# Performance work log

Hardware: AMD Instinct MI355X
Metric: run time of the kernel (lower is better)

Reference implementation:

```python
import jax, jax.numpy as jnp
import numpy as np

T, B, C = 2048, 8, 512
OUT = 512
NE = 16
TOPK = 2
LOSS_SCALE = 0.01
NEG_INF = 1.0e6  # module uses -1000000.0 for masked logits


def setup_inputs() -> dict:
    key = jax.random.key(0)
    k = jax.random.split(key, 4)
    a_assign = np.sqrt(6.0 / (C + NE)).astype(np.float32)  # xavier_uniform for Linear(C, NE)
    a_w1 = np.float32(np.sqrt(6.0) / (C + OUT))            # dynamic_init_method == 1
    return {
        "x": jax.random.normal(k[0], (T, B, C), dtype=jnp.float32),
        "assign_w": jax.random.uniform(k[1], (NE, C), minval=-a_assign, maxval=a_assign, dtype=jnp.float32),
        "assign_b": jnp.zeros((NE,), dtype=jnp.float32),
        "pw_w1": jax.random.uniform(k[2], (NE, OUT * C), minval=-a_w1, maxval=a_w1, dtype=jnp.float32),
        "bias_w": jnp.zeros((OUT, C), dtype=jnp.float32),  # pw_bias weight initialized to 0
        "bias_b": jnp.zeros((OUT,), dtype=jnp.float32),
    }


def reference(x, assign_w, assign_b, pw_w1, bias_w, bias_b):
    # key=None path of ConditionalDLFactorized18.forward, eval mode, tau=0 -> softmax gating.
    tokens = x.reshape(T * B, C)
    # Gating energies: Linear(key_dim, ne)
    energies = tokens @ assign_w.T + assign_b  # [TB, ne]
    # keeptopk_masked: set entries below k-th largest to -1e6
    topv, _ = jax.lax.top_k(energies, TOPK)
    energies = jnp.where(energies < topv[..., TOPK - 1:TOPK], -NEG_INF, energies)
    resp = jax.nn.softmax(energies, axis=-1)  # [TB, ne]
    # Importance/commitment loss (torch.std is unbiased -> ddof=1)
    importance = resp.sum(axis=0)  # [ne]
    loss = (LOSS_SCALE * jnp.std(importance, ddof=1) / jnp.mean(importance)).reshape(1)
    # Algebraically-equivalent reorder of (resp @ pw_w1).view(T,B,out,in) @ x:
    # apply each expert's matrix to the token first, then mix with resp.
    W = pw_w1.reshape(NE, OUT, C)
    expert_out = jnp.einsum("nc,eoc->neo", tokens, W)      # [TB, ne, out]
    y = jnp.einsum("ne,neo->no", resp, expert_out)          # [TB, out]
    y = y.reshape(T, B, OUT)
    # dynamic bias: pw_bias(x0) = x0 @ bias_w.T + bias_b
    y = y + x @ bias_w.T + bias_b
    return y, loss
```

## Files before the change

### kernel.cpp

```cpp
#include <hip/hip_runtime.h>
#include <hip/hip_bf16.h>

#define TB 16384
#define CDIM 512
#define OUTD 512
#define NE 16
#define NE_TOT 17
#define LOSS_SCALE 0.01f
#define BM 256
#define BN 128
#define BK 32
#define NSTEP 16
#define MAX_SCHED 80
#define MAXFLAG 8192
#define MARGIN 1e-3f

typedef __bf16 bf16_t;
typedef bf16_t bf16x8 __attribute__((ext_vector_type(8)));
typedef float f32x4 __attribute__((ext_vector_type(4)));
typedef unsigned short ushort4_t __attribute__((ext_vector_type(4)));
typedef unsigned short ushort8_t __attribute__((ext_vector_type(8)));

__device__ __forceinline__ unsigned short f2bf(float f) {
    unsigned int u = __float_as_uint(f);
    u += 0x7fffu + ((u >> 16) & 1u);
    return (unsigned short)(u >> 16);
}
__device__ __forceinline__ float bf2f(unsigned short h) {
    return __uint_as_float((unsigned int)h << 16);
}
__device__ __forceinline__ int sw4(int r) { return (r ^ (r >> 2)) & 3; }

__device__ __forceinline__ void async_copy16(void* lds, const void* g) {
    __builtin_amdgcn_global_load_lds(
        (const __attribute__((address_space(1))) unsigned int*)g,
        (__attribute__((address_space(3))) unsigned int*)lds, 16, 0, 0);
}

__global__ __launch_bounds__(256) void k_prep(
    const float* __restrict__ aw, unsigned short* __restrict__ awhl,
    int* cnt0, int* cnt1, float* importance, int* nflag, int* wflag)
{
    int t = threadIdx.x;
    if (t < NE) { cnt0[t] = 0; cnt1[t] = 0; importance[t] = 0.f; }
    if (t == 0) { *nflag = 0; *wflag = 0; }
    for (int i = t; i < NE * CDIM; i += 256) {
        float f = aw[i];
        unsigned short h = f2bf(f);
        float r = f - bf2f(h);
        awhl[i] = h;
        awhl[NE * CDIM + i] = f2bf(r);
    }
}

__global__ void k_wconv(const float* __restrict__ pw, const float* __restrict__ bw,
                        unsigned short* __restrict__ wbf, int* __restrict__ wflag) {
    long i = (long)blockIdx.x * 256 + threadIdx.x;
    const long NPW = (long)NE * OUTD * CDIM / 4;
    const long NTOT = (long)NE_TOT * OUTD * CDIM / 4;
    if (i >= NTOT) return;
    const float* src = (i < NPW) ? (pw + i * 4) : (bw + (i - NPW) * 4);
    float4 v = *(const float4*)src;
    ushort4_t o;
    o[0] = f2bf(v.x); o[1] = f2bf(v.y); o[2] = f2bf(v.z); o[3] = f2bf(v.w);
    long row = i >> 7;
    int e0 = (int)(i & 127) * 4;
    int kt = e0 >> 5;
    int cc = (e0 >> 3) & 3;
    int half = e0 & 7;
    int ccs = cc ^ sw4((int)(row & 15));
    *(ushort4_t*)(wbf + row * CDIM + kt * 32 + ccs * 8 + half) = o;
    if (i >= NPW && (v.x != 0.f || v.y != 0.f || v.z != 0.f || v.w != 0.f))
        atomicOr(wflag, 1);
}

__global__ __launch_bounds__(256) void k_gate(
    const float* __restrict__ x, const unsigned short* __restrict__ awhl,
    const float* __restrict__ ab, unsigned short* __restrict__ xbf,
    int* __restrict__ dec, float2* __restrict__ respd,
    int* __restrict__ flaglist, int* __restrict__ nflag, float* __restrict__ importance,
    int* __restrict__ cnt0, int* __restrict__ cnt1)
{
    __shared__ float imp_s[NE];
    __shared__ int c0_s[NE], c1_s[NE];
    int tid = threadIdx.x;
    if (tid < NE) { imp_s[tid] = 0.f; c0_s[tid] = 0; c1_s[tid] = 0; }
    __syncthreads();

    int wv = tid >> 6, l = tid & 63;
    int n0 = blockIdx.x * 64 + wv * 16;
    int e = l & 15;
    int kg = l >> 4;

    const float* xrow = x + (size_t)(n0 + e) * CDIM + kg * 8;
    unsigned short* xbrow = xbf + (size_t)(n0 + e) * CDIM + kg * 8;
    const unsigned short* whiP = awhl + e * CDIM + kg * 8;
    const unsigned short* wloP = whiP + NE * CDIM;

    f32x4 acc = (f32x4){0.f, 0.f, 0.f, 0.f};
    #pragma unroll 4
    for (int ks = 0; ks < 16; ++ks) {
        float4 v0 = *(const float4*)(xrow + ks * 32);
        float4 v1 = *(const float4*)(xrow + ks * 32 + 4);
        ushort8_t hx, lx;
        #define CVT(idx, f) { unsigned short h_ = f2bf(f); hx[idx] = h_; \
                              float r_ = (f) - bf2f(h_); lx[idx] = f2bf(r_); }
        CVT(0, v0.x) CVT(1, v0.y) CVT(2, v0.z) CVT(3, v0.w)
        CVT(4, v1.x) CVT(5, v1.y) CVT(6, v1.z) CVT(7, v1.w)
        #undef CVT
        *(ushort8_t*)(xbrow + ks * 32) = hx;
        ushort8_t wh8 = *(const ushort8_t*)(whiP + ks * 32);
        ushort8_t wl8 = *(const ushort8_t*)(wloP + ks * 32);
        bf16x8 ah = *(bf16x8*)&hx, al = *(bf16x8*)&lx;
        bf16x8 bh = *(bf16x8*)&wh8, bl = *(bf16x8*)&wl8;
        acc = __builtin_amdgcn_mfma_f32_16x16x32_bf16(al, bh, acc, 0, 0, 0);
        acc = __builtin_amdgcn_mfma_f32_16x16x32_bf16(ah, bl, acc, 0, 0, 0);
        acc = __builtin_amdgcn_mfma_f32_16x16x32_bf16(ah, bh, acc, 0, 0, 0);
    }
    float bias = ab[e];
    f32x4 E;
    #pragma unroll
    for (int q = 0; q < 4; ++q) E[q] = acc[q] + bias;

    f32x4 m1 = E, m2, m3;
    #pragma unroll
    for (int q = 0; q < 4; ++q) { m2[q] = -3.4e38f; m3[q] = -3.4e38f; }
    #pragma unroll
    for (int off = 1; off <= 8; off <<= 1) {
        #pragma unroll
        for (int q = 0; q < 4; ++q) {
            float o1 = __shfl_xor(m1[q], off, 64);
            float o2 = __shfl_xor(m2[q], off, 64);
            float o3 = __shfl_xor(m3[q], off, 64);
            float M1 = fmaxf(m1[q], o1), x1 = fminf(m1[q], o1);
            float h2 = fmaxf(m2[q], o2), l2 = fminf(m2[q], o2);
            float M2 = fmaxf(x1, h2), x2 = fminf(x1, h2);
            float M3 = fmaxf(fmaxf(x2, l2), fmaxf(m3[q], o3));
            m1[q] = M1; m2[q] = M2; m3[q] = M3;
        }
    }
    f32x4 p, z;
    #pragma unroll
    for (int q = 0; q < 4; ++q) p[q] = (E[q] >= m2[q]) ? expf(E[q] - m1[q]) : 0.f;
    z = p;
    #pragma unroll
    for (int off = 1; off <= 8; off <<= 1)
        #pragma unroll
        for (int q = 0; q < 4; ++q) z[q] += __shfl_xor(z[q], off, 64);
    f32x4 resp;
    #pragma unroll
    for (int q = 0; q < 4; ++q) resp[q] = p[q] / z[q];

    int grp = l >> 4;
    int elo_q[4], ehi_q[4];
    float rlo_q[4], rhi_q[4];
    #pragma unroll
    for (int q = 0; q < 4; ++q) {
        unsigned long long mq = __ballot(p[q] > 0.f);
        unsigned int sub = (unsigned int)((mq >> (grp * 16)) & 0xffffULL);
        elo_q[q] = __builtin_ctz(sub);
        ehi_q[q] = 31 - __builtin_clz(sub);
        rlo_q[q] = __shfl(resp[q], grp * 16 + elo_q[q], 64);
        rhi_q[q] = __shfl(resp[q], grp * 16 + ehi_q[q], 64);
    }
    if ((l & 15) == 0) {
        #pragma unroll
        for (int q = 0; q < 4; ++q) {
            int n = n0 + grp * 4 + q;
            dec[n] = elo_q[q] | (ehi_q[q] << 8);
            respd[n] = make_float2(rlo_q[q], rhi_q[q]);
            atomicAdd(&c0_s[elo_q[q]], 1);
            atomicAdd(&c1_s[ehi_q[q]], 1);
            if (m2[q] - m3[q] < MARGIN) {
                int ix = atomicAdd(nflag, 1);
                if (ix < MAXFLAG) flaglist[ix] = n;
            }
        }
    }
    float s = resp[0] + resp[1] + resp[2] + resp[3];
    s += __shfl_xor(s, 16, 64);
    s += __shfl_xor(s, 32, 64);
    if (l < 16) atomicAdd(&imp_s[e], s);
    __syncthreads();
    if (tid < NE) {
        unsafeAtomicAdd(&importance[tid], imp_s[tid]);
        if (c0_s[tid]) atomicAdd(&cnt0[tid], c0_s[tid]);
        if (c1_s[tid]) atomicAdd(&cnt1[tid], c1_s[tid]);
    }
}

__global__ __launch_bounds__(256) void k_repair(
    const float* __restrict__ x, const float* __restrict__ aw, const float* __restrict__ ab,
    const int* __restrict__ flaglist, const int* __restrict__ nflag,
    int* __restrict__ dec, float2* __restrict__ respd, float* __restrict__ importance,
    int* __restrict__ cnt0, int* __restrict__ cnt1)
{
    __shared__ double part[16][17];
    __shared__ double Ed[16];
    int tid = threadIdx.x;
    int e = tid >> 4, p = tid & 15;
    int nf = *nflag; if (nf > MAXFLAG) nf = MAXFLAG;
    for (int fi = blockIdx.x; fi < nf; fi += gridDim.x) {
        int n = flaglist[fi];
        const float* xp_ = x + (size_t)n * CDIM + p * 32;
        const float* wp = aw + e * CDIM + p * 32;
        double acc = 0.0;
        for (int j = 0; j < 32; ++j) acc = fma((double)xp_[j], (double)wp[j], acc);
        part[e][p] = acc;
        __syncthreads();
        if (tid < 16) {
            double s = (double)ab[tid];
            for (int q = 0; q < 16; ++q) s += part[tid][q];
            Ed[tid] = s;
        }
        __syncthreads();
        if (tid == 0) {
            double m1 = -1e300, m2 = -1e300, m3 = -1e300;
            for (int q = 0; q < 16; ++q) {
                double v = Ed[q];
                if (v > m1) { m3 = m2; m2 = m1; m1 = v; }
                else if (v > m2) { m3 = m2; m2 = v; }
                else if (v > m3) { m3 = v; }
            }
            int elo = -1, ehi = -1;
            for (int q = 0; q < 16; ++q)
                if (Ed[q] >= m2) { if (elo < 0) elo = q; else ehi = q; }
            double plo = exp(Ed[elo] - m1), phi = exp(Ed[ehi] - m1);
            double zz = plo + phi;
            float rlo = (float)(plo / zz), rhi = (float)(phi / zz);
            int od = dec[n]; float2 orr = respd[n];
            int oelo = od & 0xff, oehi = (od >> 8) & 0xff;
            unsafeAtomicAdd(&importance[oelo], -orr.x);
            unsafeAtomicAdd(&importance[oehi], -orr.y);
            unsafeAtomicAdd(&importance[elo], rlo);
            unsafeAtomicAdd(&importance[ehi], rhi);
            if (oelo != elo) { atomicSub(&cnt0[oelo], 1); atomicAdd(&cnt0[elo], 1); }
            if (oehi != ehi) { atomicSub(&cnt1[oehi], 1); atomicAdd(&cnt1[ehi], 1); }
            dec[n] = elo | (ehi << 8);
            respd[n] = make_float2(rlo, rhi);
        }
        __syncthreads();
    }
}

__global__ void k_finish(const float* __restrict__ importance, float* __restrict__ out_loss,
                         const int* __restrict__ cnt0, const int* __restrict__ cnt1,
                         int* __restrict__ fill0, int* __restrict__ fill1,
                         int* __restrict__ end0a, int* __restrict__ end1a,
                         int* __restrict__ sched0, int* __restrict__ sched1,
                         int* __restrict__ sn0, int* __restrict__ sn1) {
    int l = threadIdx.x;
    if (l < 64) {
        float v = (l < NE) ? importance[l] : 0.f;
        float s = v;
        #pragma unroll
        for (int off = 8; off >= 1; off >>= 1) s += __shfl_xor(s, off, 64);
        float mean = s / 16.f;
        float d = (l < NE) ? (v - mean) : 0.f;
        float ss = d * d;
        #pragma unroll
        for (int off = 8; off >= 1; off >>= 1) ss += __shfl_xor(ss, off, 64);
        if (l == 0) {
            float stdv = sqrtf(ss / 15.f);
            out_loss[0] = LOSS_SCALE * stdv / mean;
        }
    } else if (l == 64) {
        int p = 0, base = 0;
        for (int e = 0; e < NE; ++e) {
            fill0[e] = base;
            end0a[e] = base + cnt0[e];
            int nb = (cnt0[e] + BM - 1) / BM;
            for (int i = 0; i < nb; ++i) sched0[p++] = (e << 20) | (base + i * BM);
            base += cnt0[e];
        }
        *sn0 = p;
    } else if (l == 65) {
        int p = 0, base = 0;
        for (int e = 0; e < NE; ++e) {
            fill1[e] = base;
            end1a[e] = base + cnt1[e];
            int nb = (cnt1[e] + BM - 1) / BM;
            for (int i = 0; i < nb; ++i) sched1[p++] = (e << 20) | (base + i * BM);
            base += cnt1[e];
        }
        *sn1 = p;
    }
}

__global__ __launch_bounds__(256) void k_scatter(
    const int* __restrict__ dec, int* __restrict__ fill0, int* __restrict__ fill1,
    int* __restrict__ idx0c, int* __restrict__ idx1c)
{
    __shared__ int l0[NE], l1[NE], b0[NE], b1[NE];
    int tid = threadIdx.x;
    if (tid < NE) { l0[tid] = 0; l1[tid] = 0; }
    __syncthreads();
    int n = blockIdx.x * 256 + tid;
    int d = dec[n];
    int elo = d & 0xff, ehi = (d >> 8) & 0xff;
    int p0 = atomicAdd(&l0[elo], 1);
    int p1 = atomicAdd(&l1[ehi], 1);
    __syncthreads();
    if (tid < NE) {
        b0[tid] = atomicAdd(&fill0[tid], l0[tid]);
        b1[tid] = atomicAdd(&fill1[tid], l1[tid]);
    }
    __syncthreads();
    idx0c[b0[elo] + p0] = n;
    idx1c[b1[ehi] + p1] = n;
}

template<int MODE>
__global__ __launch_bounds__(512) void k_gemm(
    const unsigned short* __restrict__ xbf, const unsigned short* __restrict__ wbf,
    const int* __restrict__ idxc, const float2* __restrict__ respd,
    const int* __restrict__ sched, const int* __restrict__ sn,
    const int* __restrict__ enda, const int* __restrict__ wflag,
    const float* __restrict__ bias_b, float* __restrict__ y)
{
    int e, m0, end;
    if (MODE == 2) {
        if (*wflag == 0) return;
        e = NE; m0 = blockIdx.x * BM; end = TB;
    } else {
        if ((int)blockIdx.x >= *sn) return;
        int s = sched[blockIdx.x];
        e = s >> 20; m0 = s & 0xFFFFF; end = enda[e];
    }
    int n0 = blockIdx.y * BN;
    int tid = threadIdx.x;
    int wave = tid >> 6, lane = tid & 63;
    int wm = wave >> 1, wn = wave & 1;
    int fr = lane & 15, fq = lane >> 4;

    __shared__ unsigned short As[2][BM * BK];
    __shared__ unsigned short Bs[2][BN * BK];

    f32x4 acc[4][4];
    #pragma unroll
    for (int m = 0; m < 4; ++m)
        #pragma unroll
        for (int nn = 0; nn < 4; ++nn) acc[m][nn] = (f32x4){0.f, 0.f, 0.f, 0.f};

    int rl = lane >> 2, cc = lane & 3;
    const unsigned short* aS[2];
    #pragma unroll
    for (int c = 0; c < 2; ++c) {
        int rloc = wave * 32 + c * 16 + rl;
        int tokr;
        if (MODE == 2) tokr = m0 + rloc;
        else { int rr = m0 + rloc; if (rr >= end) rr = end - 1; tokr = idxc[rr]; }
        aS[c] = xbf + (size_t)tokr * CDIM + (cc ^ sw4(rloc)) * 8;
    }
    const unsigned short* bS =
        wbf + ((size_t)e * OUTD + n0 + wave * 16 + rl) * CDIM + cc * 8;

    auto stage = [&](int buf, int t) {
        async_copy16(&As[buf][(wave * 32) * BK], aS[0] + t * BK);
        async_copy16(&As[buf][(wave * 32 + 16) * BK], aS[1] + t * BK);
        async_copy16(&Bs[buf][(wave * 16) * BK], bS + t * BK);
    };
    auto compute = [&](int cb) {
        bf16x8 af[4], bv[4];
        #pragma unroll
        for (int m = 0; m < 4; ++m) {
            int row = wm * 64 + m * 16 + fr;
            af[m] = *(const bf16x8*)(&As[cb][row * BK + ((fq ^ sw4(fr)) * 8)]);
        }
        #pragma unroll
        for (int nn = 0; nn < 4; ++nn) {
            int row = wn * 64 + nn * 16 + fr;
            bv[nn] = *(const bf16x8*)(&Bs[cb][row * BK + ((fq ^ sw4(fr)) * 8)]);
        }
        #pragma unroll
        for (int m = 0; m < 4; ++m)
            #pragma unroll
            for (int nn = 0; nn < 4; ++nn)
                acc[m][nn] = __builtin_amdgcn_mfma_f32_16x16x32_bf16(af[m], bv[nn], acc[m][nn], 0, 0, 0);
    };

    stage(0, 0); stage(1, 1);
    #pragma unroll
    for (int t = 0; t < NSTEP; ++t) {
        if (t < NSTEP - 1) asm volatile("s_waitcnt vmcnt(3)" ::: "memory");
        else               asm volatile("s_waitcnt vmcnt(0)" ::: "memory");
        __builtin_amdgcn_sched_barrier(0);
        __builtin_amdgcn_s_barrier();
        asm volatile("" ::: "memory");
        compute(t & 1);
        __builtin_amdgcn_s_barrier();
        asm volatile("" ::: "memory");
        if (t + 2 < NSTEP) stage(t & 1, t + 2);
    }

    float bb[4];
    if (MODE == 0) {
        #pragma unroll
        for (int nn = 0; nn < 4; ++nn) bb[nn] = bias_b[n0 + wn * 64 + nn * 16 + fr];
    }
    #pragma unroll
    for (int m = 0; m < 4; ++m)
        #pragma unroll
        for (int q = 0; q < 4; ++q) {
            int r = m0 + wm * 64 + m * 16 + fq * 4 + q;
            if (r < end) {
                int tok = (MODE == 2) ? r : idxc[r];
                float w = 1.f;
                if (MODE != 2) {
                    float2 rp = respd[tok];
                    w = (MODE == 0) ? rp.x : rp.y;
                }
                float* yrow = y + (size_t)tok * OUTD + n0 + wn * 64 + fr;
                #pragma unroll
                for (int nn = 0; nn < 4; ++nn) {
                    if (MODE == 0)      yrow[nn * 16] = fmaf(w, acc[m][nn][q], bb[nn]);
                    else if (MODE == 1) yrow[nn * 16] += w * acc[m][nn][q];
                    else                yrow[nn * 16] += acc[m][nn][q];
                }
            }
        }
}

extern "C" void kernel_launch(void* const* d_in, const int* in_sizes, int n_in,
                              void* d_out, int out_size, void* d_ws, size_t ws_size,
                              hipStream_t stream) {
    const float* x        = (const float*)d_in[0];
    const float* assign_w = (const float*)d_in[1];
    const float* assign_b = (const float*)d_in[2];
    const float* pw_w1    = (const float*)d_in[3];
    const float* bias_w   = (const float*)d_in[4];
    const float* bias_b   = (const float*)d_in[5];
    float* y    = (float*)d_out;
    float* loss = y + (size_t)TB * OUTD;

    char* ws = (char*)d_ws;
    unsigned short* wbf  = (unsigned short*)(ws);
    unsigned short* xbf  = (unsigned short*)(ws + 8912896);
    int*    idx0c     = (int*)   (ws + 25690112);
    int*    idx1c     = (int*)   (ws + 25755648);
    int*    dec       = (int*)   (ws + 25821184);
    float2* respd     = (float2*)(ws + 25886720);
    int*    flaglist  = (int*)   (ws + 26017792);
    unsigned short* awhl = (unsigned short*)(ws + 26050560);
    char*   misc      = ws + 26083328;
    int*    cnt0      = (int*)   (misc + 0);
    int*    cnt1      = (int*)   (misc + 64);
    int*    fill0     = (int*)   (misc + 128);
    int*    fill1     = (int*)   (misc + 192);
    int*    end0a     = (int*)   (misc + 256);
    int*    end1a     = (int*)   (misc + 320);
    float*  importance= (float*) (misc + 384);
    int*    nflag     = (int*)   (misc + 448);
    int*    wflag     = (int*)   (misc + 452);
    int*    sn0       = (int*)   (misc + 456);
    int*    sn1       = (int*)   (misc + 460);
    int*    sched0    = (int*)   (misc + 512);
    int*    sched1    = (int*)   (misc + 832);

    k_prep<<<1, 256, 0, stream>>>(assign_w, awhl, cnt0, cnt1, importance, nflag, wflag);
    k_wconv<<<(NE_TOT * OUTD * CDIM / 4 + 255) / 256, 256, 0, stream>>>(pw_w1, bias_w, wbf, wflag);
    k_gate<<<TB / 64, 256, 0, stream>>>(x, awhl, assign_b, xbf, dec, respd,
                                        flaglist, nflag, importance, cnt0, cnt1);
    k_repair<<<32, 256, 0, stream>>>(x, assign_w, assign_b, flaglist, nflag,
                                     dec, respd, importance, cnt0, cnt1);
    k_finish<<<1, 128, 0, stream>>>(importance, loss, cnt0, cnt1, fill0, fill1,
                                    end0a, end1a, sched0, sched1, sn0, sn1);
    k_scatter<<<TB / 256, 256, 0, stream>>>(dec, fill0, fill1, idx0c, idx1c);
    k_gemm<0><<<dim3(MAX_SCHED, OUTD / BN), 512, 0, stream>>>(
        xbf, wbf, idx0c, respd, sched0, sn0, end0a, wflag, bias_b, y);
    k_gemm<1><<<dim3(MAX_SCHED, OUTD / BN), 512, 0, stream>>>(
        xbf, wbf, idx1c, respd, sched1, sn1, end1a, wflag, bias_b, y);
    k_gemm<2><<<dim3(TB / BM, OUTD / BN), 512, 0, stream>>>(
        xbf, wbf, idx1c, respd, sched1, sn1, end1a, wflag, bias_b, y);
}
```

Before: 111.5 us.

## Fuse top-1 and top-2 expert GEMMs into one launch with atomic ordering

Replaces the two separate grouped-GEMM launches (first and second routed expert) with one kernel. Blocks alternate between the two ranks. Second-rank blocks compute their tile and then spin on a global counter until every first-rank block has written its output, and only then do their read-modify-write accumulate. This lets the two GEMM phases overlap and removes one launch and its tail. The dense bias GEMM moves into its own specialised kernel. The risks are idle spinning blocks holding compute units, and possible deadlock if waiting blocks fill every slot before all first-rank blocks are scheduled.

Measured after the change: 299.9 us. +169.1%, slower.

```diff
diff --git a/kernel.cpp b/kernel.cpp
--- a/kernel.cpp
+++ b/kernel.cpp
@@ -39,11 +39,11 @@
 
 __global__ __launch_bounds__(256) void k_prep(
     const float* __restrict__ aw, unsigned short* __restrict__ awhl,
-    int* cnt0, int* cnt1, float* importance, int* nflag, int* wflag)
+    int* cnt0, int* cnt1, float* importance, int* nflag, int* wflag, int* done0)
 {
     int t = threadIdx.x;
     if (t < NE) { cnt0[t] = 0; cnt1[t] = 0; importance[t] = 0.f; }
-    if (t == 0) { *nflag = 0; *wflag = 0; }
+    if (t == 0) { *nflag = 0; *wflag = 0; *done0 = 0; }
     for (int i = t; i < NE * CDIM; i += 256) {
         float f = aw[i];
         unsigned short h = f2bf(f);
@@ -310,23 +310,24 @@
     idx1c[b1[ehi] + p1] = n;
 }
 
-template<int MODE>
-__global__ __launch_bounds__(512) void k_gemm(
+__global__ __launch_bounds__(512) void k_moe(
     const unsigned short* __restrict__ xbf, const unsigned short* __restrict__ wbf,
-    const int* __restrict__ idxc, const float2* __restrict__ respd,
-    const int* __restrict__ sched, const int* __restrict__ sn,
-    const int* __restrict__ enda, const int* __restrict__ wflag,
-    const float* __restrict__ bias_b, float* __restrict__ y)
+    const int* __restrict__ idx0c, const int* __restrict__ idx1c,
+    const float2* __restrict__ respd,
+    const int* __restrict__ sched0, const int* __restrict__ sched1,
+    const int* __restrict__ sn0, const int* __restrict__ sn1,
+    const int* __restrict__ end0a, const int* __restrict__ end1a,
+    const float* __restrict__ bias_b, float* __restrict__ y, int* __restrict__ done0)
 {
-    int e, m0, end;
-    if (MODE == 2) {
-        if (*wflag == 0) return;
-        e = NE; m0 = blockIdx.x * BM; end = TB;
-    } else {
-        if ((int)blockIdx.x >= *sn) return;
-        int s = sched[blockIdx.x];
-        e = s >> 20; m0 = s & 0xFFFFF; end = enda[e];
-    }
+    int rank = blockIdx.x & 1;
+    int six = blockIdx.x >> 1;
+    const int* sched = rank ? sched1 : sched0;
+    const int* idxc  = rank ? idx1c  : idx0c;
+    const int* enda  = rank ? end1a  : end0a;
+    int sn = rank ? *sn1 : *sn0;
+    if (six >= sn) return;
+    int s = sched[six];
+    int e = s >> 20, m0 = s & 0xFFFFF, end = enda[e];
     int n0 = blockIdx.y * BN;
     int tid = threadIdx.x;
     int wave = tid >> 6, lane = tid & 63;
@@ -347,10 +348,8 @@
     #pragma unroll
     for (int c = 0; c < 2; ++c) {
         int rloc = wave * 32 + c * 16 + rl;
-        int tokr;
-        if (MODE == 2) tokr = m0 + rloc;
-        else { int rr = m0 + rloc; if (rr >= end) rr = end - 1; tokr = idxc[rr]; }
-        aS[c] = xbf + (size_t)tokr * CDIM + (cc ^ sw4(rloc)) * 8;
+        int rr = m0 + rloc; if (rr >= end) rr = end - 1;
+        aS[c] = xbf + (size_t)idxc[rr] * CDIM + (cc ^ sw4(rloc)) * 8;
     }
     const unsigned short* bS =
         wbf + ((size_t)e * OUTD + n0 + wave * 16 + rl) * CDIM + cc * 8;
@@ -393,31 +392,130 @@
         if (t + 2 < NSTEP) stage(t & 1, t + 2);
     }
 
-    float bb[4];
-    if (MODE == 0) {
+    if (rank == 0) {
+        float bb[4];
         #pragma unroll
         for (int nn = 0; nn < 4; ++nn) bb[nn] = bias_b[n0 + wn * 64 + nn * 16 + fr];
-    }
+        #pragma unroll
+        for (int m = 0; m < 4; ++m)
+            #pragma unroll
+            for (int q = 0; q < 4; ++q) {
+                int r = m0 + wm * 64 + m * 16 + fq * 4 + q;
+                if (r < end) {
+                    int tok = idxc[r];
+                    float w = respd[tok].x;
+                    float* yrow = y + (size_t)tok * OUTD + n0 + wn * 64 + fr;
+                    #pragma unroll
+                    for (int nn = 0; nn < 4; ++nn)
+                        yrow[nn * 16] = fmaf(w, acc[m][nn][q], bb[nn]);
+                }
+            }
+        __threadfence();
+        __syncthreads();
+        if (tid == 0)
+            __hip_atomic_fetch_add(done0, 1, __ATOMIC_RELEASE, __HIP_MEMORY_SCOPE_AGENT);
+    } else {
+        if (tid == 0) {
+            int need = *sn0 * 4;
+            while (__hip_atomic_load(done0, __ATOMIC_ACQUIRE, __HIP_MEMORY_SCOPE_AGENT) < need)
+                __builtin_amdgcn_s_sleep(8);
+        }
+        __syncthreads();
+        #pragma unroll
+        for (int m = 0; m < 4; ++m)
+            #pragma unroll
+            for (int q = 0; q < 4; ++q) {
+                int r = m0 + wm * 64 + m * 16 + fq * 4 + q;
+                if (r < end) {
+                    int tok = idxc[r];
+                    float w = respd[tok].y;
+                    float* yrow = y + (size_t)tok * OUTD + n0 + wn * 64 + fr;
+                    #pragma unroll
+                    for (int nn = 0; nn < 4; ++nn)
+                        yrow[nn * 16] += w * acc[m][nn][q];
+                }
+            }
+    }
+}
+
+__global__ __launch_bounds__(512) void k_dense(
+    const unsigned short* __restrict__ xbf, const unsigned short* __restrict__ wbf,
+    const int* __restrict__ wflag, float* __restrict__ y)
+{
+    if (*wflag == 0) return;
+    int e = NE;
+    int m0 = blockIdx.x * BM;
+    int n0 = blockIdx.y * BN;
+    int tid = threadIdx.x;
+    int wave = tid >> 6, lane = tid & 63;
+    int wm = wave >> 1, wn = wave & 1;
+    int fr = lane & 15, fq = lane >> 4;
+
+    __shared__ unsigned short As[2][BM * BK];
+    __shared__ unsigned short Bs[2][BN * BK];
+
+    f32x4 acc[4][4];
+    #pragma unroll
+    for (int m = 0; m < 4; ++m)
+        #pragma unroll
+        for (int nn = 0; nn < 4; ++nn) acc[m][nn] = (f32x4){0.f, 0.f, 0.f, 0.f};
+
+    int rl = lane >> 2, cc = lane & 3;
+    const unsigned short* aS[2];
+    #pragma unroll
+    for (int c = 0; c < 2; ++c) {
+        int rloc = wave * 32 + c * 16 + rl;
+        aS[c] = xbf + (size_t)(m0 + rloc) * CDIM + (cc ^ sw4(rloc)) * 8;
+    }
+    const unsigned short* bS =
+        wbf + ((size_t)e * OUTD + n0 + wave * 16 + rl) * CDIM + cc * 8;
+
+    auto stage = [&](int buf, int t) {
+        async_copy16(&As[buf][(wave * 32) * BK], aS[0] + t * BK);
+        async_copy16(&As[buf][(wave * 32 + 16) * BK], aS[1] + t * BK);
+        async_copy16(&Bs[buf][(wave * 16) * BK], bS + t * BK);
+    };
+    auto compute = [&](int cb) {
+        bf16x8 af[4], bv[4];
+        #pragma unroll
+        for (int m = 0; m < 4; ++m) {
+            int row = wm * 64 + m * 16 + fr;
+            af[m] = *(const bf16x8*)(&As[cb][row * BK + ((fq ^ sw4(fr)) * 8)]);
+        }
+        #pragma unroll
+        for (int nn = 0; nn < 4; ++nn) {
+            int row = wn * 64 + nn * 16 + fr;
+            bv[nn] = *(const bf16x8*)(&Bs[cb][row * BK + ((fq ^ sw4(fr)) * 8)]);
+        }
+        #pragma unroll
+        for (int m = 0; m < 4; ++m)
+            #pragma unroll
+            for (int nn = 0; nn < 4; ++nn)
+                acc[m][nn] = __builtin_amdgcn_mfma_f32_16x16x32_bf16(af[m], bv[nn], acc[m][nn], 0, 0, 0);
+    };
+
+    stage(0, 0); stage(1, 1);
+    #pragma unroll
+    for (int t = 0; t < NSTEP; ++t) {
+        if (t < NSTEP - 1) asm volatile("s_waitcnt vmcnt(3)" ::: "memory");
+        else               asm volatile("s_waitcnt vmcnt(0)" ::: "memory");
+        __builtin_amdgcn_sched_barrier(0);
+        __builtin_amdgcn_s_barrier();
+        asm volatile("" ::: "memory");
+        compute(t & 1);
+        __builtin_amdgcn_s_barrier();
+        asm volatile("" ::: "memory");
+        if (t + 2 < NSTEP) stage(t & 1, t + 2);
+    }
+
     #pragma unroll
     for (int m = 0; m < 4; ++m)
         #pragma unroll
         for (int q = 0; q < 4; ++q) {
             int r = m0 + wm * 64 + m * 16 + fq * 4 + q;
-            if (r < end) {
-                int tok = (MODE == 2) ? r : idxc[r];
-                float w = 1.f;
-                if (MODE != 2) {
-                    float2 rp = respd[tok];
-                    w = (MODE == 0) ? rp.x : rp.y;
-                }
-                float* yrow = y + (size_t)tok * OUTD + n0 + wn * 64 + fr;
-                #pragma unroll
-                for (int nn = 0; nn < 4; ++nn) {
-                    if (MODE == 0)      yrow[nn * 16] = fmaf(w, acc[m][nn][q], bb[nn]);
-                    else if (MODE == 1) yrow[nn * 16] += w * acc[m][nn][q];
-                    else                yrow[nn * 16] += acc[m][nn][q];
-                }
-            }
+            float* yrow = y + (size_t)r * OUTD + n0 + wn * 64 + fr;
+            #pragma unroll
+            for (int nn = 0; nn < 4; ++nn) yrow[nn * 16] += acc[m][nn][q];
         }
 }
 
@@ -454,10 +552,11 @@
     int*    wflag     = (int*)   (misc + 452);
     int*    sn0       = (int*)   (misc + 456);
     int*    sn1       = (int*)   (misc + 460);
+    int*    done0     = (int*)   (misc + 464);
     int*    sched0    = (int*)   (misc + 512);
     int*    sched1    = (int*)   (misc + 832);
 
-    k_prep<<<1, 256, 0, stream>>>(assign_w, awhl, cnt0, cnt1, importance, nflag, wflag);
+    k_prep<<<1, 256, 0, stream>>>(assign_w, awhl, cnt0, cnt1, importance, nflag, wflag, done0);
     k_wconv<<<(NE_TOT * OUTD * CDIM / 4 + 255) / 256, 256, 0, stream>>>(pw_w1, bias_w, wbf, wflag);
     k_gate<<<TB / 64, 256, 0, stream>>>(x, awhl, assign_b, xbf, dec, respd,
                                         flaglist, nflag, importance, cnt0, cnt1);
@@ -466,10 +565,8 @@
     k_finish<<<1, 128, 0, stream>>>(importance, loss, cnt0, cnt1, fill0, fill1,
                                     end0a, end1a, sched0, sched1, sn0, sn1);
     k_scatter<<<TB / 256, 256, 0, stream>>>(dec, fill0, fill1, idx0c, idx1c);
-    k_gemm<0><<<dim3(MAX_SCHED, OUTD / BN), 512, 0, stream>>>(
-        xbf, wbf, idx0c, respd, sched0, sn0, end0a, wflag, bias_b, y);
-    k_gemm<1><<<dim3(MAX_SCHED, OUTD / BN), 512, 0, stream>>>(
-        xbf, wbf, idx1c, respd, sched1, sn1, end1a, wflag, bias_b, y);
-    k_gemm<2><<<dim3(TB / BM, OUTD / BN), 512, 0, stream>>>(
-        xbf, wbf, idx1c, respd, sched1, sn1, end1a, wflag, bias_b, y);
-}
+    k_moe<<<dim3(2 * MAX_SCHED, OUTD / BN), 512, 0, stream>>>(
+        xbf, wbf, idx0c, idx1c, respd, sched0, sched1, sn0, sn1,
+        end0a, end1a, bias_b, y, done0);
+    k_dense<<<dim3(TB / BM, OUTD / BN), 512, 0, stream>>>(xbf, wbf, wflag, y);
+}
```
